# Kernel tuning notes

Hardware: AMD Instinct MI355X
Metric: run time of the kernel (lower is better)

The kernel has to match this reference:

```python
import jax, jax.numpy as jnp
import numpy as np

NUM_BLOCKS = 16  # 4x4 grid of 2x2 blocks over the 8x8 matrix
E_BLK, H_BLK = 4, 2
E_CROSS, H_CROSS = 64, 8
VOCAB = 32000
LN_EPS = 1e-5


def _mha(x, Wqkv, bqkv, Wo, bo, nheads):
    """torch nn.MultiheadAttention (batch_first, self-attn, eval mode).
    Returns (out [B,T,E], attn weights averaged over heads [B,T,T])."""
    B, T, E = x.shape
    Dh = E // nheads
    qkv = x @ Wqkv.T + bqkv                      # [B,T,3E]
    q, k, v = jnp.split(qkv, 3, axis=-1)
    sp = lambda t: t.reshape(B, T, nheads, Dh).transpose(0, 2, 1, 3)  # [B,H,T,Dh]
    q, k, v = sp(q), sp(k), sp(v)
    scale = 1.0 / float(np.sqrt(Dh))
    scores = jnp.einsum('bhqd,bhkd->bhqk', q, k) * scale
    attn = jax.nn.softmax(scores, axis=-1)
    out = jnp.einsum('bhqk,bhkd->bhqd', attn, v).transpose(0, 2, 1, 3).reshape(B, T, E)
    return out @ Wo.T + bo, attn.mean(axis=1)


def _layernorm(x, g, b):
    mu = x.mean(-1, keepdims=True)
    var = x.var(-1, keepdims=True)
    return (x - mu) * jax.lax.rsqrt(var + LN_EPS) * g + b


def _to_blocks(M):
    # [B,T,8,8] -> [B,T,16,4]; block i = (row_blk*4+col_blk), 2x2 flattened row-major
    B, T = M.shape[:2]
    return jnp.transpose(M.reshape(B, T, 4, 2, 4, 2), (0, 1, 2, 4, 3, 5)).reshape(B, T, 16, 4)


def _from_blocks(x):
    # [B,T,16,4] -> [B,T,8,8]
    B, T = x.shape[:2]
    return jnp.transpose(x.reshape(B, T, 4, 4, 2, 2), (0, 1, 2, 4, 3, 5)).reshape(B, T, 8, 8)


def setup_inputs() -> dict:
    key = jax.random.key(0)
    ks = jax.random.split(key, 24)
    B, T = 4, 1024
    s = 0.05
    return {
        'M': jax.random.normal(ks[0], (B, T, 8, 8), jnp.float32),
        'token_ids': jax.random.randint(ks[1], (B, T), 0, VOCAB, jnp.int64),
        # 16 per-block MHA param sets (stacked)
        'Wqkv_blk': jax.random.normal(ks[2], (NUM_BLOCKS, 3 * E_BLK, E_BLK), jnp.float32) * s,
        'bqkv_blk': jnp.zeros((NUM_BLOCKS, 3 * E_BLK), jnp.float32),
        'Wo_blk': jax.random.normal(ks[3], (NUM_BLOCKS, E_BLK, E_BLK), jnp.float32) * s,
        'bo_blk': jnp.zeros((NUM_BLOCKS, E_BLK), jnp.float32),
        # cross-block MHA
        'Wqkv_c': jax.random.normal(ks[4], (3 * E_CROSS, E_CROSS), jnp.float32) * s,
        'bqkv_c': jnp.zeros((3 * E_CROSS,), jnp.float32),
        'Wo_c': jax.random.normal(ks[5], (E_CROSS, E_CROSS), jnp.float32) * s,
        'bo_c': jnp.zeros((E_CROSS,), jnp.float32),
        # FFN 64 -> 256 -> 64
        'W1': jax.random.normal(ks[6], (256, 64), jnp.float32) * s,
        'b1': jnp.zeros((256,), jnp.float32),
        'W2': jax.random.normal(ks[7], (64, 256), jnp.float32) * s,
        'b2': jnp.zeros((64,), jnp.float32),
        # LayerNorms
        'g1': jnp.ones((64,), jnp.float32), 'be1': jnp.zeros((64,), jnp.float32),
        'g2': jnp.ones((64,), jnp.float32), 'be2': jnp.zeros((64,), jnp.float32),
        # DynamicBlockSensitivity params
        'sens_emb': jax.random.normal(ks[8], (VOCAB, NUM_BLOCKS), jnp.float32) * s,
        'sens_alpha': jax.random.normal(ks[9], (NUM_BLOCKS,), jnp.float32) * s,
    }


def reference(M, token_ids, Wqkv_blk, bqkv_blk, Wo_blk, bo_blk,
              Wqkv_c, bqkv_c, Wo_c, bo_c, W1, b1, W2, b2,
              g1, be1, g2, be2, sens_emb, sens_alpha):
    B, T = M.shape[:2]
    blocks = _to_blocks(M)                                # [B,T,16,4]
    x_blk = jnp.moveaxis(blocks, 2, 0)                    # [16,B,T,4]
    blk_out, _ = jax.vmap(lambda x, W, b, Wo, bo: _mha(x, W, b, Wo, bo, H_BLK))(
        x_blk, Wqkv_blk, bqkv_blk, Wo_blk, bo_blk)        # [16,B,T,4]
    all_blocks = jnp.moveaxis(blk_out, 0, 2).reshape(B, T, 64)
    cross_out, attn_w = _mha(all_blocks, Wqkv_c, bqkv_c, Wo_c, bo_c, H_CROSS)
    all_blocks = _layernorm(all_blocks + cross_out, g1, be1)
    ffn = jax.nn.gelu(all_blocks @ W1.T + b1, approximate=False) @ W2.T + b2
    all_blocks = _layernorm(all_blocks + ffn, g2, be2)
    # Dynamic block sensitivity: token embedding + attention-received modulation
    attn_recv = attn_w.mean(axis=1)                       # [B,T] attention each token receives
    sens = jax.nn.sigmoid(sens_emb[token_ids] + attn_recv[..., None] * sens_alpha)  # [B,T,16]
    new_blocks = blocks + (all_blocks.reshape(B, T, 16, 4) - blocks) * sens[..., None]
    return _from_blocks(new_blocks)
```

## Files before the change

### kernel.cpp

```cpp
#include <hip/hip_runtime.h>
#include <hip/hip_bf16.h>
#include <math.h>

#define BB 4
#define TT 1024
#define BT 4096

#define OFF_BLOCKS 0
#define OFF_QKVB   262144
#define OFF_RECVP  262144
#define OFF_ALLB   1048576
#define OFF_QKVC   1310720
#define OFF_LC     2097152
#define OFF_ACCC   2129920
#define OFF_LN1    2396160
#define OFF_PARAMS 2658304
#define WS_FLOATS  2708624

#define P_W1T    0
#define P_W2T    16384
#define P_WQCT   32768
#define P_WOCT   45056
#define P_WOBLK  49152
#define P_BOBLK  49408
#define P_BQC    49472
#define P_BOC    49664
#define P_G1     49728
#define P_BE1    49792
#define P_B1     49856
#define P_B2     50112
#define P_G2     50176
#define P_BE2    50240
#define P_SAL    50304
#define P_TOTAL  50320

__device__ inline float rcpf(float x) { return __builtin_amdgcn_rcpf(x); }

__device__ inline bool detect_bf16(const void* M) {
  const unsigned short* h = (const unsigned short*)M;
  unsigned short v = h[threadIdx.x & 63];
  int e = (v >> 7) & 0xff;
  unsigned long long m = __ballot((e >= 90) && (e <= 141));
  return __popcll(m) >= 58;
}

template <bool ISBF>
__device__ inline float ldf(const void* p, int i) {
  if (ISBF) return __bfloat162float(((const __hip_bfloat16*)p)[i]);
  else      return ((const float*)p)[i];
}

template <bool ISBF>
__global__ void __launch_bounds__(256) k_prep2(
    const void* __restrict__ M,
    const void* __restrict__ Wqkv_blk,
    const void* __restrict__ bqkv_blk,
    const void* __restrict__ W1, const void* __restrict__ W2,
    const void* __restrict__ Wqkv_c, const void* __restrict__ Wo_c,
    const void* __restrict__ Wo_blk, const void* __restrict__ bo_blk,
    const void* __restrict__ bqkv_c, const void* __restrict__ bo_c,
    const void* __restrict__ g1, const void* __restrict__ be1,
    const void* __restrict__ b1, const void* __restrict__ b2,
    const void* __restrict__ g2, const void* __restrict__ be2,
    const void* __restrict__ sens_al,
    float* __restrict__ blocks, float* __restrict__ qkv_blk,
    float* __restrict__ params) {
  if (detect_bf16(M) != ISBF) return;
  if (blockIdx.x < 256) {
    int g = blockIdx.x * 256 + threadIdx.x;
    int i = g >> 12, bt = g & 4095;
    int rb = i >> 2, cb = i & 3;
    float x[4];
    #pragma unroll
    for (int r = 0; r < 2; ++r)
      #pragma unroll
      for (int c = 0; c < 2; ++c)
        x[r*2+c] = ldf<ISBF>(M, bt*64 + (rb*2+r)*8 + cb*2 + c);
    float* bo = blocks + bt*64 + i*4;
    #pragma unroll
    for (int j = 0; j < 4; ++j) bo[j] = x[j];
    float* o = qkv_blk + (i*BT + bt) * 12;
    #pragma unroll
    for (int c = 0; c < 12; ++c) {
      float a = ldf<ISBF>(bqkv_blk, i*12 + c);
      #pragma unroll
      for (int j = 0; j < 4; ++j) a += ldf<ISBF>(Wqkv_blk, i*48 + c*4 + j) * x[j];
      o[c] = a;
    }
  } else {
    for (int o = (blockIdx.x - 256)*256 + threadIdx.x; o < P_TOTAL; o += 16*256) {
      float v;
      if      (o < 16384) { int j = o >> 8, h2 = o & 255; v = ldf<ISBF>(W1, h2*64 + j); }
      else if (o < 32768) { int q = o - 16384; int k = q >> 6, j = q & 63; v = ldf<ISBF>(W2, j*256 + k); }
      else if (o < 45056) { int q = o - 32768; int j = q / 192, c = q % 192; v = ldf<ISBF>(Wqkv_c, c*64 + j); }
      else if (o < 49152) { int q = o - 45056; int m = q >> 6, j = q & 63; v = ldf<ISBF>(Wo_c, j*64 + m); }
      else if (o < 49408) v = ldf<ISBF>(Wo_blk, o - 49152);
      else if (o < 49472) v = ldf<ISBF>(bo_blk, o - 49408);
      else if (o < 49664) v = ldf<ISBF>(bqkv_c, o - 49472);
      else if (o < 49728) v = ldf<ISBF>(bo_c,   o - 49664);
      else if (o < 49792) v = ldf<ISBF>(g1,     o - 49728);
      else if (o < 49856) v = ldf<ISBF>(be1,    o - 49792);
      else if (o < 50112) v = ldf<ISBF>(b1,     o - 49856);
      else if (o < 50176) v = ldf<ISBF>(b2,     o - 50112);
      else if (o < 50240) v = ldf<ISBF>(g2,     o - 50176);
      else if (o < 50304) v = ldf<ISBF>(be2,    o - 50240);
      else                v = ldf<ISBF>(sens_al, o - 50304);
      params[o] = v;
    }
  }
}

__global__ void __launch_bounds__(512) k_blk_part(
    const float* __restrict__ qkv_blk,
    const float* __restrict__ params,
    float* __restrict__ all_blocks) {
  __shared__ float4 kv4[3072];
  __shared__ float red[128*49];
  float* kv = (float*)kv4;
  int bid = blockIdx.x;
  int qt = bid & 7, b = (bid >> 3) & 3, i = bid >> 5;
  int tid = threadIdx.x;
  int wv = __builtin_amdgcn_readfirstlane(tid) >> 6;
  int ql = tid & 63;
  const float4* slab = (const float4*)(qkv_blk + (size_t)(i*BT + b*TT) * 12);
  #pragma unroll
  for (int s = 0; s < 6; ++s) kv4[tid + s*512] = slab[tid + s*512];
  __syncthreads();
  int qa = qt*128 + ql, qb = qa + 64;
  const float* qra = kv + qa*12;
  const float* qrb = kv + qb*12;
  const float S2 = 0.70710678f;
  float qa00 = qra[0]*S2, qa01 = qra[1]*S2, qa10 = qra[2]*S2, qa11 = qra[3]*S2;
  float qb00 = qrb[0]*S2, qb01 = qrb[1]*S2, qb10 = qrb[2]*S2, qb11 = qrb[3]*S2;
  float la0=0.f, la1=0.f, aa00=0.f, aa01=0.f, aa10=0.f, aa11=0.f;
  float lb0=0.f, lb1=0.f, ab00=0.f, ab01=0.f, ab10=0.f, ab11=0.f;
  int kbeg = wv*128;
  #pragma unroll 4
  for (int k = kbeg; k < kbeg + 128; ++k) {
    const float* kr = kv + k*12 + 4;
    float k0=kr[0], k1=kr[1], k2=kr[2], k3=kr[3];
    float v0=kr[4], v1=kr[5], v2=kr[6], v3=kr[7];
    float pa0 = __expf(qa00*k0 + qa01*k1);
    float pa1 = __expf(qa10*k2 + qa11*k3);
    float pb0 = __expf(qb00*k0 + qb01*k1);
    float pb1 = __expf(qb10*k2 + qb11*k3);
    la0 += pa0; aa00 += pa0*v0; aa01 += pa0*v1;
    la1 += pa1; aa10 += pa1*v2; aa11 += pa1*v3;
    lb0 += pb0; ab00 += pb0*v0; ab01 += pb0*v1;
    lb1 += pb1; ab10 += pb1*v2; ab11 += pb1*v3;
  }
  float* ra = red + ql*49 + wv*6;
  ra[0]=la0; ra[1]=la1; ra[2]=aa00; ra[3]=aa01; ra[4]=aa10; ra[5]=aa11;
  float* rb = red + (ql+64)*49 + wv*6;
  rb[0]=lb0; rb[1]=lb1; rb[2]=ab00; rb[3]=ab01; rb[4]=ab10; rb[5]=ab11;
  __syncthreads();
  if (tid < 128) {
    float s[6] = {0.f,0.f,0.f,0.f,0.f,0.f};
    #pragma unroll
    for (int w = 0; w < 8; ++w) {
      const float* p = red + tid*49 + w*6;
      #pragma unroll
      for (int c = 0; c < 6; ++c) s[c] += p[c];
    }
    float r0 = rcpf(s[0]), r1 = rcpf(s[1]);
    float o[4] = { s[2]*r0, s[3]*r0, s[4]*r1, s[5]*r1 };
    int q2 = qt*128 + tid;
    const float* pWo = params + P_WOBLK + i*16;
    float* outp = all_blocks + (size_t)(b*TT + q2)*64 + i*4;
    #pragma unroll
    for (int j = 0; j < 4; ++j) {
      float a = params[P_BOBLK + i*4 + j];
      #pragma unroll
      for (int m2 = 0; m2 < 4; ++m2) a += pWo[j*4 + m2] * o[m2];
      outp[j] = a;
    }
  }
}

__global__ void __launch_bounds__(256) k_qkv_c2(
    const float* __restrict__ all_blocks,
    const float* __restrict__ params,
    float* __restrict__ qkv_c) {
  __shared__ float w[12288];
  __shared__ float xs[256];
  int tid = threadIdx.x;
  int t0 = blockIdx.x * 4;
  {
    const float4* src = (const float4*)(params + P_WQCT);
    float4* dst = (float4*)w;
    #pragma unroll
    for (int i = tid; i < 3072; i += 256) dst[i] = src[i];
  }
  xs[tid] = all_blocks[t0*64 + tid];
  __syncthreads();
  int tt = tid >> 6, lane = tid & 63;
  int t = t0 + tt;
  const float* x = xs + tt*64;
  float a0 = params[P_BQC + lane];
  float a1 = params[P_BQC + 64 + lane];
  float a2 = params[P_BQC + 128 + lane];
  #pragma unroll 8
  for (int j = 0; j < 64; ++j) {
    const float* r = w + j*192;
    float xj = x[j];
    a0 += r[lane]       * xj;
    a1 += r[64 + lane]  * xj;
    a2 += r[128 + lane] * xj;
  }
  float* o = qkv_c + (size_t)t*192;
  o[lane] = a0; o[64 + lane] = a1; o[128 + lane] = a2;
}

__global__ void __launch_bounds__(1024) k_cross8(
    const float* __restrict__ qkv_c,
    float* __restrict__ acc_c,
    float* __restrict__ recv_part) {
  __shared__ __align__(16) float kv[28288];
  int bid = blockIdx.x;
  int qt = bid & 7, h = (bid >> 3) & 7, b = bid >> 6;
  int tid = threadIdx.x;
  int wv = __builtin_amdgcn_readfirstlane(tid) >> 6;
  int ql = tid & 63;
  int h8 = h*8;
  const float* base = qkv_c + (size_t)b*TT*192;
  {
    int r = tid;
    const float4* kp = (const float4*)(base + (size_t)r*192 + 64 + h8);
    const float4* vp = (const float4*)(base + (size_t)r*192 + 128 + h8);
    float4 k0 = kp[0], k1 = kp[1], v0 = vp[0], v1 = vp[1];
    float4* kd = (float4*)(kv + r*8);        kd[0] = k0; kd[1] = k1;
    float4* vd = (float4*)(kv + 8192 + r*8); vd[0] = v0; vd[1] = v1;
  }
  int qa = qt*128 + ql, qb = qa + 64;
  const float SC = 0.35355339f;
  float4 qa0, qa1, qb0, qb1;
  {
    const float4* pa = (const float4*)(base + (size_t)qa*192 + h8);
    const float4* pb = (const float4*)(base + (size_t)qb*192 + h8);
    qa0 = pa[0]; qa1 = pa[1]; qb0 = pb[0]; qb1 = pb[1];
    qa0.x*=SC; qa0.y*=SC; qa0.z*=SC; qa0.w*=SC;
    qa1.x*=SC; qa1.y*=SC; qa1.z*=SC; qa1.w*=SC;
    qb0.x*=SC; qb0.y*=SC; qb0.z*=SC; qb0.w*=SC;
    qb1.x*=SC; qb1.y*=SC; qb1.z*=SC; qb1.w*=SC;
  }
  __syncthreads();
  float la = 0.f, lb = 0.f, aca[8], acb[8];
  #pragma unroll
  for (int c = 0; c < 8; ++c) { aca[c] = 0.f; acb[c] = 0.f; }
  int kbeg = wv*64;
  #pragma unroll 2
  for (int k = kbeg; k < kbeg + 64; ++k) {
    const float4* kr4 = (const float4*)(kv + k*8);
    const float4* vr4 = (const float4*)(kv + 8192 + k*8);
    float4 k0 = kr4[0], k1 = kr4[1];
    float4 v0 = vr4[0], v1 = vr4[1];
    float sa = qa0.x*k0.x + qa0.y*k0.y + qa0.z*k0.z + qa0.w*k0.w
             + qa1.x*k1.x + qa1.y*k1.y + qa1.z*k1.z + qa1.w*k1.w;
    float sb = qb0.x*k0.x + qb0.y*k0.y + qb0.z*k0.z + qb0.w*k0.w
             + qb1.x*k1.x + qb1.y*k1.y + qb1.z*k1.z + qb1.w*k1.w;
    float pa = __expf(sa);
    float pb = __expf(sb);
    la += pa; lb += pb;
    aca[0] += pa*v0.x; aca[1] += pa*v0.y; aca[2] += pa*v0.z; aca[3] += pa*v0.w;
    aca[4] += pa*v1.x; aca[5] += pa*v1.y; aca[6] += pa*v1.z; aca[7] += pa*v1.w;
    acb[0] += pb*v0.x; acb[1] += pb*v0.y; acb[2] += pb*v0.z; acb[3] += pb*v0.w;
    acb[4] += pb*v1.x; acb[5] += pb*v1.y; acb[6] += pb*v1.z; acb[7] += pb*v1.w;
  }
  __syncthreads();
  float* red  = kv + 8192;
  float* qbuf = kv + 26752;
  {
    float* ra = red + ql*145 + wv*9;
    ra[0] = la;
    #pragma unroll
    for (int c = 0; c < 8; ++c) ra[1+c] = aca[c];
    float* rb = red + (ql+64)*145 + wv*9;
    rb[0] = lb;
    #pragma unroll
    for (int c = 0; c < 8; ++c) rb[1+c] = acb[c];
    if (wv == 0) {
      float4* qd = (float4*)(qbuf + ql*12);
      qd[0] = qa0; qd[1] = qa1;
      float4* qd2 = (float4*)(qbuf + (ql+64)*12);
      qd2[0] = qb0; qd2[1] = qb1;
    }
  }
  __syncthreads();
  if (tid < 128) {
    float ls = 0.f, as[8];
    #pragma unroll
    for (int c = 0; c < 8; ++c) as[c] = 0.f;
    #pragma unroll
    for (int w = 0; w < 16; ++w) {
      const float* p = red + tid*145 + w*9;
      ls += p[0];
      #pragma unroll
      for (int c = 0; c < 8; ++c) as[c] += p[1+c];
    }
    float invl = rcpf(ls);
    int q2 = qt*128 + tid;
    int idx = (b*8 + h)*TT + q2;
    float4 o0 = { as[0]*invl, as[1]*invl, as[2]*invl, as[3]*invl };
    float4 o1 = { as[4]*invl, as[5]*invl, as[6]*invl, as[7]*invl };
    float4* op = (float4*)(acc_c + (size_t)idx*8);
    op[0] = o0; op[1] = o1;
    qbuf[tid*12 + 8] = invl;
  }
  __syncthreads();
  {
    int qh = wv >> 3, g = wv & 7;
    int p = g*64 + ql;
    float K0[8], K1[8];
    {
      const float4* a  = (const float4*)(kv + p*8);
      const float4* b2 = (const float4*)(kv + (p+512)*8);
      float4 t0 = a[0],  t1 = a[1];
      float4 t2 = b2[0], t3 = b2[1];
      K0[0]=t0.x;K0[1]=t0.y;K0[2]=t0.z;K0[3]=t0.w;K0[4]=t1.x;K0[5]=t1.y;K0[6]=t1.z;K0[7]=t1.w;
      K1[0]=t2.x;K1[1]=t2.y;K1[2]=t2.z;K1[3]=t2.w;K1[4]=t3.x;K1[5]=t3.y;K1[6]=t3.z;K1[7]=t3.w;
    }
    float r0 = 0.f, r1 = 0.f;
    const float* qb0p = qbuf + qh*64*12;
    #pragma unroll 4
    for (int qq = 0; qq < 64; ++qq) {
      const float* qr = qb0p + qq*12;
      float4 q0 = *(const float4*)qr;
      float4 q1 = *(const float4*)(qr + 4);
      float invl = qr[8];
      float s0 = q0.x*K0[0]+q0.y*K0[1]+q0.z*K0[2]+q0.w*K0[3]
               + q1.x*K0[4]+q1.y*K0[5]+q1.z*K0[6]+q1.w*K0[7];
      float s1 = q0.x*K1[0]+q0.y*K1[1]+q0.z*K1[2]+q0.w*K1[3]
               + q1.x*K1[4]+q1.y*K1[5]+q1.z*K1[6]+q1.w*K1[7];
      r0 += __expf(s0) * invl;
      r1 += __expf(s1) * invl;
    }
    int src = h*16 + qt*2 + qh;
    recv_part[((size_t)(b*1024 + p      ))*128 + src] = r0;
    recv_part[((size_t)(b*1024 + p + 512))*128 + src] = r1;
  }
}

__global__ void __launch_bounds__(256) k_fin(
    const float* __restrict__ all_blocks,
    const float* __restrict__ acc_c,
    const float* __restrict__ params,
    float* __restrict__ ln1) {
  __shared__ float pvs[4*64];
  int tt = threadIdx.x >> 6, j = threadIdx.x & 63;
  int t = blockIdx.x*4 + tt;
  int b = t >> 10, tl = t & 1023;
  int h = j >> 3;
  int idx = (b*8 + h)*TT + tl;
  pvs[tt*64 + j] = acc_c[idx*8 + (j & 7)];
  __syncthreads();
  float a = params[P_BOC + j];
  const float* WoT = params + P_WOCT;
  const float* p = pvs + tt*64;
  #pragma unroll 8
  for (int m = 0; m < 64; ++m) a += WoT[m*64 + j] * p[m];
  float x = all_blocks[t*64 + j] + a;
  float s = x, s2 = x*x;
  #pragma unroll
  for (int off = 32; off; off >>= 1) { s += __shfl_xor(s, off); s2 += __shfl_xor(s2, off); }
  float mu  = s  * (1.f/64.f);
  float var = s2 * (1.f/64.f) - mu*mu;
  float y = (x - mu) * rsqrtf(var + 1e-5f) * params[P_G1 + j] + params[P_BE1 + j];
  ln1[t*64 + j] = y;
}

template <bool ISBF>
__global__ void __launch_bounds__(512) k_ffn_out2(
    const void* __restrict__ M,
    const float* __restrict__ ln1,
    const float* __restrict__ params,
    const float* __restrict__ blocks,
    const int* __restrict__ tok32,
    const float* __restrict__ recv_part,
    const void* __restrict__ sens_emb,
    void* __restrict__ out) {
  if (detect_bf16(M) != ISBF) return;
  __shared__ float w[16384];
  __shared__ float ld2[512];
  __shared__ float hbuf[2048];
  int tid = threadIdx.x;
  int t0 = blockIdx.x * 8;
  int wv = tid >> 6, lane = tid & 63;
  float recv;
  {
    int t = t0 + wv, b = t >> 10, k = t & 1023;
    const float* rp = recv_part + ((size_t)(b*1024 + k))*128;
    float s = rp[lane] + rp[lane + 64];
    #pragma unroll
    for (int off = 32; off; off >>= 1) s += __shfl_xor(s, off);
    recv = s * (1.f/8192.f);
  }
  ld2[lane*8 + wv] = ln1[(t0 + wv)*64 + lane];
  {
    const float4* src = (const float4*)(params + P_W1T);
    float4* dst = (float4*)w;
    #pragma unroll
    for (int i = tid; i < 4096; i += 512) dst[i] = src[i];
  }
  __syncthreads();
  {
    int g = tid >> 8, u = tid & 255;
    float a0, a1, a2, a3;
    a0 = a1 = a2 = a3 = params[P_B1 + u];
    #pragma unroll 8
    for (int j = 0; j < 64; ++j) {
      float wj = w[j*256 + u];
      float4 xj = *(const float4*)(ld2 + j*8 + g*4);
      a0 += wj*xj.x; a1 += wj*xj.y; a2 += wj*xj.z; a3 += wj*xj.w;
    }
    float av[4] = {a0, a1, a2, a3};
    #pragma unroll
    for (int t2 = 0; t2 < 4; ++t2) {
      float v = av[t2];
      float u2 = 1.5957691f*v + 0.07135481f*v*v*v;
      hbuf[(g*4 + t2)*256 + u] = v * rcpf(1.f + __expf(-u2));
    }
  }
  __syncthreads();
  {
    const float4* src = (const float4*)(params + P_W2T);
    float4* dst = (float4*)w;
    #pragma unroll
    for (int i = tid; i < 4096; i += 512) dst[i] = src[i];
  }
  __syncthreads();
  int j = lane;
  int t = t0 + wv, b = t >> 10;
  float y = params[P_B2 + j];
  const float* hb = hbuf + wv*256;
  #pragma unroll 8
  for (int k = 0; k < 256; ++k) y += w[k*64 + j] * hb[k];
  float z = ld2[j*8 + wv] + y;
  float s = z, s2 = z*z;
  #pragma unroll
  for (int off = 32; off; off >>= 1) { s += __shfl_xor(s, off); s2 += __shfl_xor(s2, off); }
  float mu  = s  * (1.f/64.f);
  float var = s2 * (1.f/64.f) - mu*mu;
  float y2 = (z - mu) * rsqrtf(var + 1e-5f) * params[P_G2 + j] + params[P_BE2 + j];
  bool is64 = ((tok32[1] | tok32[3] | tok32[5] | tok32[7]) == 0);
  int tok = is64 ? tok32[t*2] : tok32[t];
  int i = j >> 2, e = j & 3;
  float sv = ldf<ISBF>(sens_emb, tok*16 + i) + recv * params[P_SAL + i];
  float sg = rcpf(1.f + __expf(-sv));
  float blk = blocks[t*64 + j];
  float nb = blk + (y2 - blk) * sg;
  int rb = i >> 2, cb = i & 3, r = e >> 1, c = e & 1;
  int oidx = t*64 + (rb*2 + r)*8 + cb*2 + c;
  if (ISBF) ((__hip_bfloat16*)out)[oidx] = __float2bfloat16(nb);
  else      ((float*)out)[oidx] = nb;
}

extern "C" void kernel_launch(void* const* d_in, const int* in_sizes, int n_in,
                              void* d_out, int out_size, void* d_ws, size_t ws_size,
                              hipStream_t stream) {
  const void* M        = d_in[0];
  const int*  tok      = (const int*)d_in[1];
  const void* Wqkv_blk = d_in[2];
  const void* bqkv_blk = d_in[3];
  const void* Wo_blk   = d_in[4];
  const void* bo_blk   = d_in[5];
  const void* Wqkv_c   = d_in[6];
  const void* bqkv_c   = d_in[7];
  const void* Wo_c     = d_in[8];
  const void* bo_c     = d_in[9];
  const void* W1       = d_in[10];
  const void* b1       = d_in[11];
  const void* W2       = d_in[12];
  const void* b2       = d_in[13];
  const void* g1       = d_in[14];
  const void* be1      = d_in[15];
  const void* g2i      = d_in[16];
  const void* be2      = d_in[17];
  const void* sens_emb = d_in[18];
  const void* sens_al  = d_in[19];

  float* ws = (float*)d_ws;
  float* blocks    = ws + OFF_BLOCKS;
  float* qkv_blk   = ws + OFF_QKVB;
  float* recv_part = ws + OFF_RECVP;
  float* all_blk   = ws + OFF_ALLB;
  float* qkv_c     = ws + OFF_QKVC;
  float* acc_c     = ws + OFF_ACCC;
  float* ln1       = ws + OFF_LN1;
  float* params    = ws + OFF_PARAMS;

  k_prep2<true ><<<272, 256, 0, stream>>>(M, Wqkv_blk, bqkv_blk, W1, W2, Wqkv_c, Wo_c,
                                          Wo_blk, bo_blk, bqkv_c, bo_c, g1, be1, b1, b2,
                                          g2i, be2, sens_al, blocks, qkv_blk, params);
  k_prep2<false><<<272, 256, 0, stream>>>(M, Wqkv_blk, bqkv_blk, W1, W2, Wqkv_c, Wo_c,
                                          Wo_blk, bo_blk, bqkv_c, bo_c, g1, be1, b1, b2,
                                          g2i, be2, sens_al, blocks, qkv_blk, params);
  k_blk_part<<<512, 512, 0, stream>>>(qkv_blk, params, all_blk);
  k_qkv_c2<<<1024, 256, 0, stream>>>(all_blk, params, qkv_c);
  k_cross8<<<256, 1024, 0, stream>>>(qkv_c, acc_c, recv_part);
  k_fin<<<1024, 256, 0, stream>>>(all_blk, acc_c, params, ln1);
  k_ffn_out2<true ><<<512, 512, 0, stream>>>(M, ln1, params, blocks, tok, recv_part,
                                             sens_emb, (void*)d_out);
  k_ffn_out2<false><<<512, 512, 0, stream>>>(M, ln1, params, blocks, tok, recv_part,
                                             sens_emb, (void*)d_out);
}
```

Baseline: 207.0 us.

## Use packed fp16 K/V and dot2 instructions in block and cross attention

Both attention kernels now store K and V in shared memory as packed fp16 pairs and compute QK scores with the v_dot2 fp32-accumulate instruction. The cross kernel also folds the softmax normalizer into the exponent as a log2 offset, using exp2 with fma, and unrolls the main loop further. The aim is to halve shared-memory footprint and load traffic and to cut the ALU work per score. In exchange, scores and values lose precision to fp16, which may shift results near tolerance.

```diff
diff --git a/kernel.cpp b/kernel.cpp
--- a/kernel.cpp
+++ b/kernel.cpp
@@ -35,6 +35,28 @@
 #define P_TOTAL  50320
 
 __device__ inline float rcpf(float x) { return __builtin_amdgcn_rcpf(x); }
+
+typedef _Float16 h2 __attribute__((ext_vector_type(2)));
+typedef __fp16   fh2 __attribute__((ext_vector_type(2)));
+
+__device__ inline uint pkh(float a, float b) {
+#if __has_builtin(__builtin_amdgcn_cvt_pkrtz)
+  fh2 r = __builtin_amdgcn_cvt_pkrtz(a, b);
+  return __builtin_bit_cast(uint, r);
+#else
+  h2 r = { (_Float16)a, (_Float16)b };
+  return __builtin_bit_cast(uint, r);
+#endif
+}
+__device__ inline h2 toh2(uint u) { return __builtin_bit_cast(h2, u); }
+
+__device__ inline float dot2h(h2 a, h2 b, float c) {
+#if __has_builtin(__builtin_amdgcn_fdot2)
+  return __builtin_amdgcn_fdot2(a, b, c, false);
+#else
+  return c + (float)a.x * (float)b.x + (float)a.y * (float)b.y;
+#endif
+}
 
 __device__ inline bool detect_bf16(const void* M) {
   const unsigned short* h = (const unsigned short*)M;
@@ -90,7 +112,7 @@
   } else {
     for (int o = (blockIdx.x - 256)*256 + threadIdx.x; o < P_TOTAL; o += 16*256) {
       float v;
-      if      (o < 16384) { int j = o >> 8, h2 = o & 255; v = ldf<ISBF>(W1, h2*64 + j); }
+      if      (o < 16384) { int j = o >> 8, h2_ = o & 255; v = ldf<ISBF>(W1, h2_*64 + j); }
       else if (o < 32768) { int q = o - 16384; int k = q >> 6, j = q & 63; v = ldf<ISBF>(W2, j*256 + k); }
       else if (o < 45056) { int q = o - 32768; int j = q / 192, c = q % 192; v = ldf<ISBF>(Wqkv_c, c*64 + j); }
       else if (o < 49152) { int q = o - 45056; int m = q >> 6, j = q & 63; v = ldf<ISBF>(Wo_c, j*64 + m); }
@@ -110,44 +132,52 @@
   }
 }
 
-__global__ void __launch_bounds__(512) k_blk_part(
+__global__ void __launch_bounds__(512) k_blk2(
     const float* __restrict__ qkv_blk,
     const float* __restrict__ params,
     float* __restrict__ all_blocks) {
-  __shared__ float4 kv4[3072];
-  __shared__ float red[128*49];
-  float* kv = (float*)kv4;
+  __shared__ __align__(16) uint lds[14464];
+  float* qf  = (float*)lds;
+  uint*  kvu = lds + 4096;
+  float* red = (float*)(lds + 8192);
   int bid = blockIdx.x;
   int qt = bid & 7, b = (bid >> 3) & 3, i = bid >> 5;
   int tid = threadIdx.x;
   int wv = __builtin_amdgcn_readfirstlane(tid) >> 6;
   int ql = tid & 63;
-  const float4* slab = (const float4*)(qkv_blk + (size_t)(i*BT + b*TT) * 12);
+  const float* slab = qkv_blk + (size_t)(i*BT + b*TT) * 12;
   #pragma unroll
-  for (int s = 0; s < 6; ++s) kv4[tid + s*512] = slab[tid + s*512];
+  for (int rr = 0; rr < 2; ++rr) {
+    int r = tid + rr*512;
+    const float4* rp = (const float4*)(slab + (size_t)r*12);
+    float4 x0 = rp[0], x1 = rp[1], x2 = rp[2];
+    *(float4*)(qf + r*4) = x0;
+    *(uint4*)(kvu + r*4) = make_uint4(pkh(x1.x,x1.y), pkh(x1.z,x1.w),
+                                      pkh(x2.x,x2.y), pkh(x2.z,x2.w));
+  }
   __syncthreads();
   int qa = qt*128 + ql, qb = qa + 64;
-  const float* qra = kv + qa*12;
-  const float* qrb = kv + qb*12;
   const float S2 = 0.70710678f;
-  float qa00 = qra[0]*S2, qa01 = qra[1]*S2, qa10 = qra[2]*S2, qa11 = qra[3]*S2;
-  float qb00 = qrb[0]*S2, qb01 = qrb[1]*S2, qb10 = qrb[2]*S2, qb11 = qrb[3]*S2;
+  float4 qav = *(const float4*)(qf + qa*4);
+  float4 qbv = *(const float4*)(qf + qb*4);
+  uint qa01 = pkh(qav.x*S2, qav.y*S2), qa23 = pkh(qav.z*S2, qav.w*S2);
+  uint qb01 = pkh(qbv.x*S2, qbv.y*S2), qb23 = pkh(qbv.z*S2, qbv.w*S2);
   float la0=0.f, la1=0.f, aa00=0.f, aa01=0.f, aa10=0.f, aa11=0.f;
   float lb0=0.f, lb1=0.f, ab00=0.f, ab01=0.f, ab10=0.f, ab11=0.f;
   int kbeg = wv*128;
   #pragma unroll 4
   for (int k = kbeg; k < kbeg + 128; ++k) {
-    const float* kr = kv + k*12 + 4;
-    float k0=kr[0], k1=kr[1], k2=kr[2], k3=kr[3];
-    float v0=kr[4], v1=kr[5], v2=kr[6], v3=kr[7];
-    float pa0 = __expf(qa00*k0 + qa01*k1);
-    float pa1 = __expf(qa10*k2 + qa11*k3);
-    float pb0 = __expf(qb00*k0 + qb01*k1);
-    float pb1 = __expf(qb10*k2 + qb11*k3);
-    la0 += pa0; aa00 += pa0*v0; aa01 += pa0*v1;
-    la1 += pa1; aa10 += pa1*v2; aa11 += pa1*v3;
-    lb0 += pb0; ab00 += pb0*v0; ab01 += pb0*v1;
-    lb1 += pb1; ab10 += pb1*v2; ab11 += pb1*v3;
+    uint4 kk = *(const uint4*)(kvu + k*4);
+    h2 k01 = toh2(kk.x), k23 = toh2(kk.y);
+    h2 v01 = toh2(kk.z), v23 = toh2(kk.w);
+    float pa0 = __expf(dot2h(toh2(qa01), k01, 0.f));
+    float pa1 = __expf(dot2h(toh2(qa23), k23, 0.f));
+    float pb0 = __expf(dot2h(toh2(qb01), k01, 0.f));
+    float pb1 = __expf(dot2h(toh2(qb23), k23, 0.f));
+    la0 += pa0; aa00 += pa0*(float)v01.x; aa01 += pa0*(float)v01.y;
+    la1 += pa1; aa10 += pa1*(float)v23.x; aa11 += pa1*(float)v23.y;
+    lb0 += pb0; ab00 += pb0*(float)v01.x; ab01 += pb0*(float)v01.y;
+    lb1 += pb1; ab10 += pb1*(float)v23.x; ab11 += pb1*(float)v23.y;
   }
   float* ra = red + ql*49 + wv*6;
   ra[0]=la0; ra[1]=la1; ra[2]=aa00; ra[3]=aa01; ra[4]=aa10; ra[5]=aa11;
@@ -211,11 +241,15 @@
   o[lane] = a0; o[64 + lane] = a1; o[128 + lane] = a2;
 }
 
-__global__ void __launch_bounds__(1024) k_cross8(
+__global__ void __launch_bounds__(1024) k_cross9(
     const float* __restrict__ qkv_c,
     float* __restrict__ acc_c,
     float* __restrict__ recv_part) {
-  __shared__ __align__(16) float kv[28288];
+  __shared__ __align__(16) uint lds[23680];
+  uint*  Ku  = lds;
+  uint*  Vu  = lds + 4096;
+  float* red = (float*)(lds + 4096);
+  uint*  qb_ = lds + 22656;
   int bid = blockIdx.x;
   int qt = bid & 7, h = (bid >> 3) & 7, b = bid >> 6;
   int tid = threadIdx.x;
@@ -228,47 +262,51 @@
     const float4* kp = (const float4*)(base + (size_t)r*192 + 64 + h8);
     const float4* vp = (const float4*)(base + (size_t)r*192 + 128 + h8);
     float4 k0 = kp[0], k1 = kp[1], v0 = vp[0], v1 = vp[1];
-    float4* kd = (float4*)(kv + r*8);        kd[0] = k0; kd[1] = k1;
-    float4* vd = (float4*)(kv + 8192 + r*8); vd[0] = v0; vd[1] = v1;
-  }
-  int qa = qt*128 + ql, qb = qa + 64;
+    *(uint4*)(Ku + r*4) = make_uint4(pkh(k0.x,k0.y), pkh(k0.z,k0.w),
+                                     pkh(k1.x,k1.y), pkh(k1.z,k1.w));
+    *(uint4*)(Vu + r*4) = make_uint4(pkh(v0.x,v0.y), pkh(v0.z,v0.w),
+                                     pkh(v1.x,v1.y), pkh(v1.z,v1.w));
+  }
+  int qa = qt*128 + ql, qbq = qa + 64;
   const float SC = 0.35355339f;
-  float4 qa0, qa1, qb0, qb1;
+  uint qa01,qa23,qa45,qa67, qb01,qb23,qb45,qb67;
   {
     const float4* pa = (const float4*)(base + (size_t)qa*192 + h8);
-    const float4* pb = (const float4*)(base + (size_t)qb*192 + h8);
-    qa0 = pa[0]; qa1 = pa[1]; qb0 = pb[0]; qb1 = pb[1];
-    qa0.x*=SC; qa0.y*=SC; qa0.z*=SC; qa0.w*=SC;
-    qa1.x*=SC; qa1.y*=SC; qa1.z*=SC; qa1.w*=SC;
-    qb0.x*=SC; qb0.y*=SC; qb0.z*=SC; qb0.w*=SC;
-    qb1.x*=SC; qb1.y*=SC; qb1.z*=SC; qb1.w*=SC;
+    const float4* pb = (const float4*)(base + (size_t)qbq*192 + h8);
+    float4 a0 = pa[0], a1 = pa[1], b0 = pb[0], b1 = pb[1];
+    qa01 = pkh(a0.x*SC, a0.y*SC); qa23 = pkh(a0.z*SC, a0.w*SC);
+    qa45 = pkh(a1.x*SC, a1.y*SC); qa67 = pkh(a1.z*SC, a1.w*SC);
+    qb01 = pkh(b0.x*SC, b0.y*SC); qb23 = pkh(b0.z*SC, b0.w*SC);
+    qb45 = pkh(b1.x*SC, b1.y*SC); qb67 = pkh(b1.z*SC, b1.w*SC);
   }
   __syncthreads();
   float la = 0.f, lb = 0.f, aca[8], acb[8];
   #pragma unroll
   for (int c = 0; c < 8; ++c) { aca[c] = 0.f; acb[c] = 0.f; }
   int kbeg = wv*64;
-  #pragma unroll 2
+  #pragma unroll 4
   for (int k = kbeg; k < kbeg + 64; ++k) {
-    const float4* kr4 = (const float4*)(kv + k*8);
-    const float4* vr4 = (const float4*)(kv + 8192 + k*8);
-    float4 k0 = kr4[0], k1 = kr4[1];
-    float4 v0 = vr4[0], v1 = vr4[1];
-    float sa = qa0.x*k0.x + qa0.y*k0.y + qa0.z*k0.z + qa0.w*k0.w
-             + qa1.x*k1.x + qa1.y*k1.y + qa1.z*k1.z + qa1.w*k1.w;
-    float sb = qb0.x*k0.x + qb0.y*k0.y + qb0.z*k0.z + qb0.w*k0.w
-             + qb1.x*k1.x + qb1.y*k1.y + qb1.z*k1.z + qb1.w*k1.w;
+    uint4 kk = *(const uint4*)(Ku + k*4);
+    uint4 vv = *(const uint4*)(Vu + k*4);
+    h2 k01 = toh2(kk.x), k23 = toh2(kk.y), k45 = toh2(kk.z), k67 = toh2(kk.w);
+    float sa = dot2h(toh2(qa01),k01, dot2h(toh2(qa23),k23,
+               dot2h(toh2(qa45),k45, dot2h(toh2(qa67),k67, 0.f))));
+    float sb = dot2h(toh2(qb01),k01, dot2h(toh2(qb23),k23,
+               dot2h(toh2(qb45),k45, dot2h(toh2(qb67),k67, 0.f))));
     float pa = __expf(sa);
     float pb = __expf(sb);
     la += pa; lb += pb;
-    aca[0] += pa*v0.x; aca[1] += pa*v0.y; aca[2] += pa*v0.z; aca[3] += pa*v0.w;
-    aca[4] += pa*v1.x; aca[5] += pa*v1.y; aca[6] += pa*v1.z; aca[7] += pa*v1.w;
-    acb[0] += pb*v0.x; acb[1] += pb*v0.y; acb[2] += pb*v0.z; acb[3] += pb*v0.w;
-    acb[4] += pb*v1.x; acb[5] += pb*v1.y; acb[6] += pb*v1.z; acb[7] += pb*v1.w;
-  }
-  __syncthreads();
-  float* red  = kv + 8192;
-  float* qbuf = kv + 26752;
+    h2 v01 = toh2(vv.x), v23 = toh2(vv.y), v45 = toh2(vv.z), v67 = toh2(vv.w);
+    aca[0] += pa*(float)v01.x; aca[1] += pa*(float)v01.y;
+    aca[2] += pa*(float)v23.x; aca[3] += pa*(float)v23.y;
+    aca[4] += pa*(float)v45.x; aca[5] += pa*(float)v45.y;
+    aca[6] += pa*(float)v67.x; aca[7] += pa*(float)v67.y;
+    acb[0] += pb*(float)v01.x; acb[1] += pb*(float)v01.y;
+    acb[2] += pb*(float)v23.x; acb[3] += pb*(float)v23.y;
+    acb[4] += pb*(float)v45.x; acb[5] += pb*(float)v45.y;
+    acb[6] += pb*(float)v67.x; acb[7] += pb*(float)v67.y;
+  }
+  __syncthreads();
   {
     float* ra = red + ql*145 + wv*9;
     ra[0] = la;
@@ -279,10 +317,8 @@
     #pragma unroll
     for (int c = 0; c < 8; ++c) rb[1+c] = acb[c];
     if (wv == 0) {
-      float4* qd = (float4*)(qbuf + ql*12);
-      qd[0] = qa0; qd[1] = qa1;
-      float4* qd2 = (float4*)(qbuf + (ql+64)*12);
-      qd2[0] = qb0; qd2[1] = qb1;
+      *(uint4*)(qb_ + ql*8)      = make_uint4(qa01, qa23, qa45, qa67);
+      *(uint4*)(qb_ + (ql+64)*8) = make_uint4(qb01, qb23, qb45, qb67);
     }
   }
   __syncthreads();
@@ -304,35 +340,28 @@
     float4 o1 = { as[4]*invl, as[5]*invl, as[6]*invl, as[7]*invl };
     float4* op = (float4*)(acc_c + (size_t)idx*8);
     op[0] = o0; op[1] = o1;
-    qbuf[tid*12 + 8] = invl;
+    ((float*)(qb_ + tid*8))[4] = -__log2f(ls);
   }
   __syncthreads();
   {
     int qh = wv >> 3, g = wv & 7;
     int p = g*64 + ql;
-    float K0[8], K1[8];
-    {
-      const float4* a  = (const float4*)(kv + p*8);
-      const float4* b2 = (const float4*)(kv + (p+512)*8);
-      float4 t0 = a[0],  t1 = a[1];
-      float4 t2 = b2[0], t3 = b2[1];
-      K0[0]=t0.x;K0[1]=t0.y;K0[2]=t0.z;K0[3]=t0.w;K0[4]=t1.x;K0[5]=t1.y;K0[6]=t1.z;K0[7]=t1.w;
-      K1[0]=t2.x;K1[1]=t2.y;K1[2]=t2.z;K1[3]=t2.w;K1[4]=t3.x;K1[5]=t3.y;K1[6]=t3.z;K1[7]=t3.w;
-    }
+    uint4 ka = *(const uint4*)(Ku + p*4);
+    uint4 kb = *(const uint4*)(Ku + (p+512)*4);
+    h2 A0 = toh2(ka.x), A1 = toh2(ka.y), A2 = toh2(ka.z), A3 = toh2(ka.w);
+    h2 B0 = toh2(kb.x), B1 = toh2(kb.y), B2 = toh2(kb.z), B3 = toh2(kb.w);
     float r0 = 0.f, r1 = 0.f;
-    const float* qb0p = qbuf + qh*64*12;
+    const uint* qrow = qb_ + qh*64*8;
+    const float L2E = 1.44269504f;
     #pragma unroll 4
     for (int qq = 0; qq < 64; ++qq) {
-      const float* qr = qb0p + qq*12;
-      float4 q0 = *(const float4*)qr;
-      float4 q1 = *(const float4*)(qr + 4);
-      float invl = qr[8];
-      float s0 = q0.x*K0[0]+q0.y*K0[1]+q0.z*K0[2]+q0.w*K0[3]
-               + q1.x*K0[4]+q1.y*K0[5]+q1.z*K0[6]+q1.w*K0[7];
-      float s1 = q0.x*K1[0]+q0.y*K1[1]+q0.z*K1[2]+q0.w*K1[3]
-               + q1.x*K1[4]+q1.y*K1[5]+q1.z*K1[6]+q1.w*K1[7];
-      r0 += __expf(s0) * invl;
-      r1 += __expf(s1) * invl;
+      uint4 q4 = *(const uint4*)(qrow + qq*8);
+      float mq = __uint_as_float(qrow[qq*8 + 4]);
+      h2 Q0 = toh2(q4.x), Q1 = toh2(q4.y), Q2 = toh2(q4.z), Q3 = toh2(q4.w);
+      float s0 = dot2h(Q0,A0, dot2h(Q1,A1, dot2h(Q2,A2, dot2h(Q3,A3, 0.f))));
+      float s1 = dot2h(Q0,B0, dot2h(Q1,B1, dot2h(Q2,B2, dot2h(Q3,B3, 0.f))));
+      r0 += exp2f(fmaf(s0, L2E, mq));
+      r1 += exp2f(fmaf(s1, L2E, mq));
     }
     int src = h*16 + qt*2 + qh;
     recv_part[((size_t)(b*1024 + p      ))*128 + src] = r0;
@@ -494,9 +523,9 @@
   k_prep2<false><<<272, 256, 0, stream>>>(M, Wqkv_blk, bqkv_blk, W1, W2, Wqkv_c, Wo_c,
                                           Wo_blk, bo_blk, bqkv_c, bo_c, g1, be1, b1, b2,
                                           g2i, be2, sens_al, blocks, qkv_blk, params);
-  k_blk_part<<<512, 512, 0, stream>>>(qkv_blk, params, all_blk);
+  k_blk2<<<512, 512, 0, stream>>>(qkv_blk, params, all_blk);
   k_qkv_c2<<<1024, 256, 0, stream>>>(all_blk, params, qkv_c);
-  k_cross8<<<256, 1024, 0, stream>>>(qkv_c, acc_c, recv_part);
+  k_cross9<<<256, 1024, 0, stream>>>(qkv_c, acc_c, recv_part);
   k_fin<<<1024, 256, 0, stream>>>(all_blk, acc_c, params, ln1);
   k_ffn_out2<true ><<<512, 512, 0, stream>>>(M, ln1, params, blocks, tok, recv_part,
                                              sens_emb, (void*)d_out);
```

Result: no change. 204.8 us (-1.1%).
